# Optimization experiments

Measured on AMD Instinct MI355X. Metric: run time of the kernel, lower is better.

## Reference

```python
import jax, jax.numpy as jnp
import numpy as np

N = 50000
E = 640000
D = 128
R = 8
LAMDA = 1


def _conv(x, row, col, edge_type, coef, W, b):
    # Transform every node by every relation weight: [N, R, D]
    xW = jnp.einsum('nd,rdo->nro', x, W)
    # Gather the per-edge transformed source feature: [E, D]
    msg = xW[row, edge_type] * coef[:, None]
    # Scatter-add to target nodes, then bias
    return jax.ops.segment_sum(msg, col, num_segments=N) + b


def setup_inputs() -> dict:
    key = jax.random.key(0)
    ks = jax.random.split(key, 8)
    x = jax.random.normal(ks[0], (N, D), dtype=jnp.float32)
    edge_index = jax.random.randint(ks[1], (2, E), 0, N, dtype=jnp.int64)
    edge_type = jax.random.randint(ks[2], (E,), 0, R, dtype=jnp.int64)
    edge_weight = jax.random.uniform(ks[3], (E,), dtype=jnp.float32)
    # kaiming_uniform_(a=sqrt(5)) on [R, D, D]: bound = sqrt(6/((1+5)*fan_in)) = 1/sqrt(fan_in)
    bound = 1.0 / np.sqrt(D)
    W1 = jax.random.uniform(ks[4], (R, D, D), minval=-bound, maxval=bound, dtype=jnp.float32)
    W2 = jax.random.uniform(ks[5], (R, D, D), minval=-bound, maxval=bound, dtype=jnp.float32)
    b1 = jnp.zeros((D,), dtype=jnp.float32)
    b2 = jnp.zeros((D,), dtype=jnp.float32)
    return {"x": x, "edge_index": edge_index, "edge_type": edge_type,
            "edge_weight": edge_weight, "W1": W1, "b1": b1, "W2": W2, "b2": b2}


def reference(x, edge_index, edge_type, edge_weight, W1, b1, W2, b2):
    row = edge_index[0]  # source nodes (x_j)
    col = edge_index[1]  # target nodes (aggregation)
    deg = jax.ops.segment_sum(jnp.ones((E,), dtype=x.dtype), col, num_segments=N)
    deg_inv_sqrt = jnp.where(deg == 0, 1.0, deg ** -0.5)
    norm = deg_inv_sqrt[row] * deg_inv_sqrt[col]
    coef = norm * edge_weight  # [E]

    z1 = jax.nn.leaky_relu(_conv(x, row, col, edge_type, coef, W1, b1), negative_slope=0.01)
    # dropout is identity in eval mode
    z2 = _conv(z1, row, col, edge_type, coef, W2, b2)

    z_star = (x + z1 + z2) / 4.0
    # z_sharp = sum(temp[LAMDA:]) / (4 - LAMDA) with temp = [x, z1, z2]
    temp = [x, z1, z2]
    z_sharp = temp[LAMDA]
    for i in range(LAMDA + 1, 3):
        z_sharp = z_sharp + temp[i]
    z_sharp = z_sharp / (4.0 - LAMDA)
    return (z_star, z_sharp)
```

## Files before the change

### kernel.cpp

```cpp
#include <hip/hip_runtime.h>
#include <hip/hip_bf16.h>

#define DD 128
#define NREL 8
#define LDHB 1032
#define BC 16

typedef float f32x4 __attribute__((ext_vector_type(4)));
typedef short short8 __attribute__((ext_vector_type(8)));

__device__ __forceinline__ float dis_f(float deg) {
    return deg == 0.0f ? 1.0f : rsqrtf(deg);
}

__global__ __launch_bounds__(256) void prep_kernel(const int* __restrict__ ei,
                                                   int* __restrict__ cnt, int E, int eb,
                                                   const float* __restrict__ x,
                                                   __hip_bfloat16* __restrict__ xb, int total4) {
    if (blockIdx.x < (unsigned)eb) {
        int e = blockIdx.x * 256 + threadIdx.x;
        if (e < E) atomicAdd(&cnt[ei[E + e]], 1);
    } else {
        int i = (blockIdx.x - eb) * 256 + threadIdx.x;
        if (i >= total4) return;
        const float4 a = ((const float4*)x)[i];
        __hip_bfloat162 p0 = __float22bfloat162_rn(make_float2(a.x, a.y));
        __hip_bfloat162 p1 = __float22bfloat162_rn(make_float2(a.z, a.w));
        uint2 u;
        u.x = *(unsigned int*)&p0;
        u.y = *(unsigned int*)&p1;
        *(uint2*)&xb[(size_t)i * 4] = u;
    }
}

__global__ __launch_bounds__(256) void scanA_kernel(const int* __restrict__ cnt,
                                                    int* __restrict__ bsum, int N) {
    __shared__ int s[256];
    const int i = blockIdx.x * 256 + threadIdx.x;
    int v = (i < N) ? ((cnt[i] + 7) & ~7) : 0;
    s[threadIdx.x] = v;
    __syncthreads();
    for (int off = 1; off < 256; off <<= 1) {
        int add = (threadIdx.x >= off) ? s[threadIdx.x - off] : 0;
        __syncthreads();
        s[threadIdx.x] += add;
        __syncthreads();
    }
    if (threadIdx.x == 255) bsum[blockIdx.x] = s[255];
}

__global__ __launch_bounds__(256) void scanB_kernel(int* __restrict__ bsum,
                                                    int* __restrict__ pstart,
                                                    int nblk, int N) {
    __shared__ int s[256];
    const int t = threadIdx.x;
    int v = (t < nblk) ? bsum[t] : 0;
    s[t] = v;
    __syncthreads();
    for (int off = 1; off < 256; off <<= 1) {
        int add = (t >= off) ? s[t - off] : 0;
        __syncthreads();
        s[t] += add;
        __syncthreads();
    }
    if (t < nblk) bsum[t] = s[t] - v;
    if (t == 255) pstart[N] = s[255];
}

__global__ __launch_bounds__(256) void scanC_kernel(const int* __restrict__ cnt,
                                                    const int* __restrict__ bsum,
                                                    int* __restrict__ pstart,
                                                    int* __restrict__ cursor,
                                                    uint2* __restrict__ ebuf, int N) {
    __shared__ int s[256];
    const int i = blockIdx.x * 256 + threadIdx.x;
    const int cn = (i < N) ? cnt[i] : 0;
    const int v = (cn + 7) & ~7;
    s[threadIdx.x] = v;
    __syncthreads();
    for (int off = 1; off < 256; off <<= 1) {
        int add = (threadIdx.x >= off) ? s[threadIdx.x - off] : 0;
        __syncthreads();
        s[threadIdx.x] += add;
        __syncthreads();
    }
    if (i < N) {
        const int excl = s[threadIdx.x] - v + bsum[blockIdx.x];
        pstart[i] = excl;
        cursor[i] = excl;
        for (int j = cn; j < v; ++j) ebuf[excl + j] = make_uint2(0u, 0u);
    }
}

__global__ __launch_bounds__(256) void bucket_kernel(const int* __restrict__ ei,
                                                     const int* __restrict__ et,
                                                     const float* __restrict__ ew,
                                                     const int* __restrict__ cnt,
                                                     int* __restrict__ cursor,
                                                     uint2* __restrict__ ebuf, int E) {
    int e = blockIdx.x * blockDim.x + threadIdx.x;
    if (e >= E) return;
    const int row = ei[e], col = ei[E + e];
    const float coef = dis_f((float)cnt[row]) * dis_f((float)cnt[col]) * ew[e];
    const int pos = atomicAdd(&cursor[col], 1);
    ebuf[pos] = make_uint2(((unsigned)et[e] << 16) | (unsigned)row, __float_as_uint(coef));
}

__global__ __launch_bounds__(256) void wtrans_kernel(const float* __restrict__ W1,
                                                     const float* __restrict__ W2,
                                                     __hip_bfloat16* __restrict__ BT1,
                                                     __hip_bfloat16* __restrict__ BT2) {
    __shared__ __hip_bfloat16 tile[128][130];
    const int r = blockIdx.x & 7;
    const float* W = (blockIdx.x >> 3) ? W2 : W1;
    __hip_bfloat16* BT = (blockIdx.x >> 3) ? BT2 : BT1;
    const int o = threadIdx.x & 127;
    const int h = threadIdx.x >> 7;
    for (int d = h; d < DD; d += 2)
        tile[d][o] = __float2bfloat16(W[((size_t)r * DD + d) * DD + o]);
    __syncthreads();
    const int d = threadIdx.x & 127;
    for (int o2 = h; o2 < DD; o2 += 2)
        BT[(size_t)o2 * 1024 + r * DD + d] = tile[d][o2];
}

template<int LAYER>
__global__ __launch_bounds__(512, 8) void fused_kernel(const __hip_bfloat16* __restrict__ srcb,
                                                       const uint2* __restrict__ ebuf,
                                                       const int* __restrict__ pstart,
                                                       const __hip_bfloat16* __restrict__ BT,
                                                       const float* __restrict__ bias,
                                                       const __hip_bfloat16* __restrict__ xbp,
                                                       __hip_bfloat16* __restrict__ z1b,
                                                       float* __restrict__ out, int N) {
    __shared__ __hip_bfloat16 hb[BC][LDHB];
    const int tid = threadIdx.x;
    const int w = tid >> 6, l = tid & 63;
    const int c0 = blockIdx.x * BC;

    #pragma unroll
    for (int q = 0; q < 2; ++q) {
        const int c = c0 + 2 * w + q;
        float acc[16];
        #pragma unroll
        for (int i = 0; i < 16; ++i) acc[i] = 0.f;
        if (c < N) {
            const int beg = __builtin_amdgcn_readfirstlane(pstart[c]);
            const int end = __builtin_amdgcn_readfirstlane(pstart[c + 1]);
            for (int e = beg; e < end; e += 8) {
                unsigned ms[8]; float cf[8]; unsigned vv[8];
                #pragma unroll
                for (int i = 0; i < 8; ++i) {
                    const uint2 rr = ebuf[e + i];
                    ms[i] = (unsigned)__builtin_amdgcn_readfirstlane((int)rr.x);
                    cf[i] = __uint_as_float((unsigned)__builtin_amdgcn_readfirstlane((int)rr.y));
                }
                #pragma unroll
                for (int i = 0; i < 8; ++i)
                    vv[i] = *(const unsigned*)&srcb[(size_t)(ms[i] & 0xffffu) * DD + 2 * l];
                #pragma unroll
                for (int i = 0; i < 8; ++i) {
                    const float xl = __uint_as_float(vv[i] << 16);
                    const float xh = __uint_as_float(vv[i] & 0xffff0000u);
                    const float cf_ = cf[i];
                    switch (ms[i] >> 16) {
                        case 0: acc[0]  += cf_*xl; acc[1]  += cf_*xh; break;
                        case 1: acc[2]  += cf_*xl; acc[3]  += cf_*xh; break;
                        case 2: acc[4]  += cf_*xl; acc[5]  += cf_*xh; break;
                        case 3: acc[6]  += cf_*xl; acc[7]  += cf_*xh; break;
                        case 4: acc[8]  += cf_*xl; acc[9]  += cf_*xh; break;
                        case 5: acc[10] += cf_*xl; acc[11] += cf_*xh; break;
                        case 6: acc[12] += cf_*xl; acc[13] += cf_*xh; break;
                        default: acc[14] += cf_*xl; acc[15] += cf_*xh; break;
                    }
                }
            }
        }
        const int m = 2 * w + q;
        #pragma unroll
        for (int r = 0; r < NREL; ++r) {
            __hip_bfloat162 p = __float22bfloat162_rn(make_float2(acc[2 * r], acc[2 * r + 1]));
            *(unsigned int*)&hb[m][r * DD + 2 * l] = *(unsigned int*)&p;
        }
    }
    __syncthreads();

    const int lk = (l >> 4) * 8;
    const int lr = l & 15;
    f32x4 acc0 = {0.f, 0.f, 0.f, 0.f};
    const __hip_bfloat16* bt = BT + (size_t)(w * 16 + lr) * 1024 + lk;
    const __hip_bfloat16* h0 = &hb[lr][lk];
    #pragma unroll 8
    for (int k0 = 0; k0 < 1024; k0 += 32) {
        const short8 b  = *(const short8*)(bt + k0);
        const short8 a0 = *(const short8*)(h0 + k0);
        acc0 = __builtin_amdgcn_mfma_f32_16x16x32_bf16(a0, b, acc0, 0, 0, 0);
    }

    const int rbase = (l >> 4) * 4;
    const int o = w * 16 + lr;
    const float bv = bias[o];
    #pragma unroll
    for (int q = 0; q < 4; ++q) {
        const int c = c0 + rbase + q;
        if (c >= N) continue;
        const size_t idx = (size_t)c * DD + o;
        float v = acc0[q] + bv;
        if (LAYER == 1) {
            v = v >= 0.f ? v : 0.01f * v;
            z1b[idx] = __float2bfloat16(v);
        } else {
            const float z1v = __bfloat162float(z1b[idx]);
            const float xv2 = __bfloat162float(xbp[idx]);
            out[idx] = (xv2 + z1v + v) * 0.25f;
            out[(size_t)N * DD + idx] = (z1v + v) * (1.f / 3.f);
        }
    }
}

extern "C" void kernel_launch(void* const* d_in, const int* in_sizes, int n_in,
                              void* d_out, int out_size, void* d_ws, size_t ws_size,
                              hipStream_t stream) {
    const float* x  = (const float*)d_in[0];
    const int*   ei = (const int*)d_in[1];
    const int*   et = (const int*)d_in[2];
    const float* ew = (const float*)d_in[3];
    const float* W1 = (const float*)d_in[4];
    const float* b1 = (const float*)d_in[5];
    const float* W2 = (const float*)d_in[6];
    const float* b2 = (const float*)d_in[7];

    const int N = in_sizes[0] / DD;
    const int E = in_sizes[3];
    float* out = (float*)d_out;

    char* w = (char*)d_ws;
    int* cnt = (int*)w;                 w += (size_t)N * 4;
    int* pstart = (int*)w;              w += (size_t)(N + 16) * 4;
    int* cursor = (int*)w;              w += (size_t)N * 4;
    int* bsum = (int*)w;                w += 256 * 4;
    __hip_bfloat16* BT1 = (__hip_bfloat16*)w;  w += (size_t)DD * NREL * DD * 2;
    __hip_bfloat16* BT2 = (__hip_bfloat16*)w;  w += (size_t)DD * NREL * DD * 2;
    uint2* ebuf = (uint2*)w;            w += ((size_t)E + 8 * (size_t)N) * 8;
    __hip_bfloat16* xb = (__hip_bfloat16*)w;   w += (size_t)N * DD * 2;
    __hip_bfloat16* z1b = (__hip_bfloat16*)w;

    hipMemsetAsync(cnt, 0, (size_t)N * 4, stream);

    const int eb = (E + 255) / 256;
    const int t4 = N * DD / 4;
    const int xblk = (t4 + 255) / 256;
    const int nscb = (N + 255) / 256;

    prep_kernel<<<eb + xblk, 256, 0, stream>>>(ei, cnt, E, eb, x, xb, t4);
    wtrans_kernel<<<16, 256, 0, stream>>>(W1, W2, BT1, BT2);
    scanA_kernel<<<nscb, 256, 0, stream>>>(cnt, bsum, N);
    scanB_kernel<<<1, 256, 0, stream>>>(bsum, pstart, nscb, N);
    scanC_kernel<<<nscb, 256, 0, stream>>>(cnt, bsum, pstart, cursor, ebuf, N);
    bucket_kernel<<<eb, 256, 0, stream>>>(ei, et, ew, cnt, cursor, ebuf, E);

    const int nb = (N + BC - 1) / BC;
    fused_kernel<1><<<nb, 512, 0, stream>>>(xb,  ebuf, pstart, BT1, b1, xb, z1b, out, N);
    fused_kernel<2><<<nb, 512, 0, stream>>>(z1b, ebuf, pstart, BT2, b2, xb, z1b, out, N);
}
```

Before: 347.0 us.

## Sub-bucket each destination's edge list by source-node window for gather locality

Edge counting and bucketing now keep eight counters per destination node, keyed by the source index shifted right by 13. Each node's CSR segment is therefore ordered by source-node range. The scan kernels sum and expand these per-window counts into sub-offsets. The aim is to make the feature gathers in the fused aggregation kernels more cache-local, at the cost of an eight-times-larger counter array, a bigger memset and more scan traffic.

```diff
diff --git a/kernel.cpp b/kernel.cpp
--- a/kernel.cpp
+++ b/kernel.cpp
@@ -5,6 +5,7 @@
 #define NREL 8
 #define LDHB 1032
 #define BC 16
+#define NW 8
 
 typedef float f32x4 __attribute__((ext_vector_type(4)));
 typedef short short8 __attribute__((ext_vector_type(8)));
@@ -14,12 +15,15 @@
 }
 
 __global__ __launch_bounds__(256) void prep_kernel(const int* __restrict__ ei,
-                                                   int* __restrict__ cnt, int E, int eb,
+                                                   int* __restrict__ wofs, int E, int eb,
                                                    const float* __restrict__ x,
                                                    __hip_bfloat16* __restrict__ xb, int total4) {
     if (blockIdx.x < (unsigned)eb) {
         int e = blockIdx.x * 256 + threadIdx.x;
-        if (e < E) atomicAdd(&cnt[ei[E + e]], 1);
+        if (e < E) {
+            const int row = ei[e], col = ei[E + e];
+            atomicAdd(&wofs[col * NW + (row >> 13)], 1);
+        }
     } else {
         int i = (blockIdx.x - eb) * 256 + threadIdx.x;
         if (i >= total4) return;
@@ -33,12 +37,18 @@
     }
 }
 
-__global__ __launch_bounds__(256) void scanA_kernel(const int* __restrict__ cnt,
+__global__ __launch_bounds__(256) void scanA_kernel(const int* __restrict__ wofs,
                                                     int* __restrict__ bsum, int N) {
     __shared__ int s[256];
     const int i = blockIdx.x * 256 + threadIdx.x;
-    int v = (i < N) ? ((cnt[i] + 7) & ~7) : 0;
-    s[threadIdx.x] = v;
+    int padded = 0;
+    if (i < N) {
+        int t = 0;
+        #pragma unroll
+        for (int k = 0; k < NW; ++k) t += wofs[i * NW + k];
+        padded = (t + 7) & ~7;
+    }
+    s[threadIdx.x] = padded;
     __syncthreads();
     for (int off = 1; off < 256; off <<= 1) {
         int add = (threadIdx.x >= off) ? s[threadIdx.x - off] : 0;
@@ -67,16 +77,21 @@
     if (t == 255) pstart[N] = s[255];
 }
 
-__global__ __launch_bounds__(256) void scanC_kernel(const int* __restrict__ cnt,
+__global__ __launch_bounds__(256) void scanC_kernel(int* __restrict__ wofs,
                                                     const int* __restrict__ bsum,
                                                     int* __restrict__ pstart,
-                                                    int* __restrict__ cursor,
+                                                    int* __restrict__ cnt,
                                                     uint2* __restrict__ ebuf, int N) {
     __shared__ int s[256];
     const int i = blockIdx.x * 256 + threadIdx.x;
-    const int cn = (i < N) ? cnt[i] : 0;
-    const int v = (cn + 7) & ~7;
-    s[threadIdx.x] = v;
+    int cw[NW];
+    int tot = 0;
+    if (i < N) {
+        #pragma unroll
+        for (int k = 0; k < NW; ++k) { cw[k] = wofs[i * NW + k]; tot += cw[k]; }
+    }
+    const int padded = (tot + 7) & ~7;
+    s[threadIdx.x] = padded;
     __syncthreads();
     for (int off = 1; off < 256; off <<= 1) {
         int add = (threadIdx.x >= off) ? s[threadIdx.x - off] : 0;
@@ -85,10 +100,13 @@
         __syncthreads();
     }
     if (i < N) {
-        const int excl = s[threadIdx.x] - v + bsum[blockIdx.x];
+        const int excl = s[threadIdx.x] - padded + bsum[blockIdx.x];
         pstart[i] = excl;
-        cursor[i] = excl;
-        for (int j = cn; j < v; ++j) ebuf[excl + j] = make_uint2(0u, 0u);
+        cnt[i] = tot;
+        int run = excl;
+        #pragma unroll
+        for (int k = 0; k < NW; ++k) { wofs[i * NW + k] = run; run += cw[k]; }
+        for (int j = tot; j < padded; ++j) ebuf[excl + j] = make_uint2(0u, 0u);
     }
 }
 
@@ -96,13 +114,13 @@
                                                      const int* __restrict__ et,
                                                      const float* __restrict__ ew,
                                                      const int* __restrict__ cnt,
-                                                     int* __restrict__ cursor,
+                                                     int* __restrict__ wofs,
                                                      uint2* __restrict__ ebuf, int E) {
     int e = blockIdx.x * blockDim.x + threadIdx.x;
     if (e >= E) return;
     const int row = ei[e], col = ei[E + e];
     const float coef = dis_f((float)cnt[row]) * dis_f((float)cnt[col]) * ew[e];
-    const int pos = atomicAdd(&cursor[col], 1);
+    const int pos = atomicAdd(&wofs[col * NW + (row >> 13)], 1);
     ebuf[pos] = make_uint2(((unsigned)et[e] << 16) | (unsigned)row, __float_as_uint(coef));
 }
 
@@ -237,7 +255,7 @@
     char* w = (char*)d_ws;
     int* cnt = (int*)w;                 w += (size_t)N * 4;
     int* pstart = (int*)w;              w += (size_t)(N + 16) * 4;
-    int* cursor = (int*)w;              w += (size_t)N * 4;
+    int* wofs = (int*)w;                w += (size_t)N * NW * 4;
     int* bsum = (int*)w;                w += 256 * 4;
     __hip_bfloat16* BT1 = (__hip_bfloat16*)w;  w += (size_t)DD * NREL * DD * 2;
     __hip_bfloat16* BT2 = (__hip_bfloat16*)w;  w += (size_t)DD * NREL * DD * 2;
@@ -245,19 +263,19 @@
     __hip_bfloat16* xb = (__hip_bfloat16*)w;   w += (size_t)N * DD * 2;
     __hip_bfloat16* z1b = (__hip_bfloat16*)w;
 
-    hipMemsetAsync(cnt, 0, (size_t)N * 4, stream);
+    hipMemsetAsync(wofs, 0, (size_t)N * NW * 4, stream);
 
     const int eb = (E + 255) / 256;
     const int t4 = N * DD / 4;
     const int xblk = (t4 + 255) / 256;
     const int nscb = (N + 255) / 256;
 
-    prep_kernel<<<eb + xblk, 256, 0, stream>>>(ei, cnt, E, eb, x, xb, t4);
+    prep_kernel<<<eb + xblk, 256, 0, stream>>>(ei, wofs, E, eb, x, xb, t4);
     wtrans_kernel<<<16, 256, 0, stream>>>(W1, W2, BT1, BT2);
-    scanA_kernel<<<nscb, 256, 0, stream>>>(cnt, bsum, N);
+    scanA_kernel<<<nscb, 256, 0, stream>>>(wofs, bsum, N);
     scanB_kernel<<<1, 256, 0, stream>>>(bsum, pstart, nscb, N);
-    scanC_kernel<<<nscb, 256, 0, stream>>>(cnt, bsum, pstart, cursor, ebuf, N);
-    bucket_kernel<<<eb, 256, 0, stream>>>(ei, et, ew, cnt, cursor, ebuf, E);
+    scanC_kernel<<<nscb, 256, 0, stream>>>(wofs, bsum, pstart, cnt, ebuf, N);
+    bucket_kernel<<<eb, 256, 0, stream>>>(ei, et, ew, cnt, wofs, ebuf, E);
 
     const int nb = (N + BC - 1) / BC;
     fused_kernel<1><<<nb, 512, 0, stream>>>(xb,  ebuf, pstart, BT1, b1, xb, z1b, out, N);
```

Result: no change. 343.7 us (-0.9%).
